# Kernel tuning notes

Hardware: AMD Instinct MI355X
Metric: run time of the kernel (lower is better)

Reference implementation:

```python
import jax, jax.numpy as jnp
import numpy as np

N_NODES_PER_SLICE = 1024  # n_physical_qubits + 1


def _gcn_layer(x, row, col, n_nodes, W, b):
    """PyG GCNConv: add self-loops, symmetric deg normalization, linear, scatter-add, +bias."""
    sl = jnp.arange(n_nodes, dtype=row.dtype)
    row_f = jnp.concatenate([row, sl])
    col_f = jnp.concatenate([col, sl])
    deg = jax.ops.segment_sum(jnp.ones_like(col_f, dtype=x.dtype), col_f, num_segments=n_nodes)
    dinv = jnp.where(deg > 0, jax.lax.rsqrt(deg), 0.0)
    norm = dinv[row_f] * dinv[col_f]            # [E_total]
    h = x @ W                                    # [n_nodes, out]
    msg = h[row_f] * norm[:, None]               # gather + scale
    out = jax.ops.segment_sum(msg, col_f, num_segments=n_nodes)  # scatter-add
    return out + b


def reference(edge_index, qubit_embeddings, W1, b1, W2, b2, W3, b3):
    B = edge_index.shape[0]
    npn = N_NODES_PER_SLICE
    n_nodes = B * npn
    # Batch.from_data_list: offset each slice's edge_index by b * npn, tile node features
    offsets = (jnp.arange(B, dtype=edge_index.dtype) * npn)[:, None]  # [B,1]
    row = (edge_index[:, 0, :] + offsets).reshape(-1)  # [B*E]
    col = (edge_index[:, 1, :] + offsets).reshape(-1)
    x = jnp.tile(qubit_embeddings, (B, 1))             # [B*npn, d0]
    for W, b in ((W1, b1), (W2, b2), (W3, b3)):
        x = jax.nn.relu(_gcn_layer(x, row, col, n_nodes, W, b))
    return x


def setup_inputs() -> dict:
    key = jax.random.key(0)
    ks = jax.random.split(key, 8)
    B, E, d = 512, 2048, 128
    return {
        "edge_index": jax.random.randint(ks[0], (B, 2, E), 0, N_NODES_PER_SLICE, dtype=jnp.int64 if jax.config.jax_enable_x64 else jnp.int32),
        "qubit_embeddings": jax.random.normal(ks[1], (N_NODES_PER_SLICE, d), dtype=jnp.float32),
        "W1": jax.random.normal(ks[2], (d, d), dtype=jnp.float32) * (1.0 / np.sqrt(d)),
        "b1": jnp.zeros((d,), dtype=jnp.float32),
        "W2": jax.random.normal(ks[3], (d, d), dtype=jnp.float32) * (1.0 / np.sqrt(d)),
        "b2": jnp.zeros((d,), dtype=jnp.float32),
        "W3": jax.random.normal(ks[4], (d, d), dtype=jnp.float32) * (1.0 / np.sqrt(d)),
        "b3": jnp.zeros((d,), dtype=jnp.float32),
    }
```

## Files before the change

### kernel.cpp

```cpp
#include <hip/hip_runtime.h>

#define NPN   1024
#define NB    512
#define NE_S  2048
#define DD    128
#define NN    (NB * NPN)
#define NE    (NB * NE_S)

typedef short s16x8 __attribute__((ext_vector_type(8)));
typedef float f32x4 __attribute__((ext_vector_type(4)));

static __device__ __forceinline__ unsigned short f2bf(float f) {
    unsigned u = __builtin_bit_cast(unsigned, f);
    unsigned r = (u + 0x7FFFu + ((u >> 16) & 1u)) >> 16;
    return (unsigned short)r;
}
static __device__ __forceinline__ float bf2f(unsigned short h) {
    unsigned u = ((unsigned)h) << 16;
    return __builtin_bit_cast(float, u);
}


__global__ void k_count(const int* __restrict__ ei, int* __restrict__ deg) {
    int t = blockIdx.x * 256 + threadIdx.x;
    int b = t >> 11, e = t & (NE_S - 1);
    int col = ei[b * (2 * NE_S) + NE_S + e];
    atomicAdd(&deg[b * NPN + col], 1);
}

__global__ void k_dinv(const int* __restrict__ deg, float* __restrict__ dinv) {
    int i = blockIdx.x * 256 + threadIdx.x;
    dinv[i] = rsqrtf((float)(deg[i] + 1));
}

__global__ __launch_bounds__(1024) void k_scan(const int* __restrict__ deg,
                                               int* __restrict__ coff,
                                               int* __restrict__ cur) {
    __shared__ int s[NPN];
    int b = blockIdx.x, t = threadIdx.x;
    int v = deg[b * NPN + t];
    s[t] = v;
    __syncthreads();
    for (int off = 1; off < NPN; off <<= 1) {
        int add = (t >= off) ? s[t - off] : 0;
        __syncthreads();
        s[t] += add;
        __syncthreads();
    }
    coff[b * NPN + t] = b * NE_S + (s[t] - v);
    cur[b * NPN + t] = 0;
}

__global__ void k_fill(const int* __restrict__ ei, const float* __restrict__ dinv,
                       const int* __restrict__ coff, int* __restrict__ cur,
                       int* __restrict__ crow, float* __restrict__ cnorm) {
    int t = blockIdx.x * 256 + threadIdx.x;
    int b = t >> 11, e = t & (NE_S - 1);
    int r = ei[b * (2 * NE_S) + e];
    int c = ei[b * (2 * NE_S) + NE_S + e];
    int gr = b * NPN + r, gc = b * NPN + c;
    int pos = coff[gc] + atomicAdd(&cur[gc], 1);
    crow[pos]  = gr;
    cnorm[pos] = dinv[gr] * dinv[gc];
}


__global__ __launch_bounds__(256) void k_wsplit(const float* __restrict__ W,
                                                short* __restrict__ WTh,
                                                short* __restrict__ WTl) {
    int idx = blockIdx.x * 256 + threadIdx.x;
    int k = idx >> 7, n = idx & 127;
    float f = W[idx];
    unsigned short h = f2bf(f);
    unsigned short l = f2bf(f - bf2f(h));
    WTh[n * DD + k] = (short)h;
    WTl[n * DD + k] = (short)l;
}


__global__ __launch_bounds__(512, 4) void k_layer(const float* __restrict__ x,
                                                  unsigned gmask,
                                                  const short* __restrict__ WTh,
                                                  const short* __restrict__ WTl,
                                                  const float* __restrict__ bias,
                                                  const float* __restrict__ dinv,
                                                  const int* __restrict__ coff,
                                                  const int* __restrict__ deg,
                                                  const int* __restrict__ crow,
                                                  const float* __restrict__ cnorm,
                                                  float* __restrict__ out) {
    __shared__ short sH[128 * DD];
    __shared__ short sL[128 * DD];

    int t = threadIdx.x;
    int wave = t >> 6, lane = t & 63;
    int wb = (int)((blockIdx.x & 7) * 512 + (blockIdx.x >> 3));
    int m0 = wb * 128;

    int n  = lane & 15;
    int kq = lane >> 4;

    const short* bhp = &WTh[(wave * 16 + n) * DD + kq * 8];
    const short* blp = &WTl[(wave * 16 + n) * DD + kq * 8];
    s16x8 bh[4], bl[4];
    #pragma unroll
    for (int ks = 0; ks < 4; ++ks) {
        bh[ks] = *(const s16x8*)(bhp + ks * 32);
        bl[ks] = *(const s16x8*)(blp + ks * 32);
    }

    for (int i = 0; i < 16; ++i) {
        int row = wave * 16 + i;
        int g = m0 + row;
        float dv = dinv[g];
        float2 v = *(const float2*)&x[(size_t)(g & gmask) * DD + lane * 2];
        float ax = dv * dv * v.x, ay = dv * dv * v.y;
        int beg = coff[g], cnt = deg[g];
        for (int e = 0; e < cnt; ++e) {
            int r = crow[beg + e];
            float nw = cnorm[beg + e];
            float2 rv = *(const float2*)&x[(size_t)(r & gmask) * DD + lane * 2];
            ax += nw * rv.x; ay += nw * rv.y;
        }
        unsigned short hx = f2bf(ax); unsigned short lx = f2bf(ax - bf2f(hx));
        unsigned short hy = f2bf(ay); unsigned short ly = f2bf(ay - bf2f(hy));
        unsigned hwrd = ((unsigned)hy << 16) | hx;
        unsigned lwrd = ((unsigned)ly << 16) | lx;
        unsigned bo = ((unsigned)row * 256u + (unsigned)lane * 4u) ^ ((unsigned)(row & 7) << 4);
        *(unsigned*)((char*)sH + bo) = hwrd;
        *(unsigned*)((char*)sL + bo) = lwrd;
    }
    __syncthreads();

    f32x4 acc[8];
    #pragma unroll
    for (int m = 0; m < 8; ++m) acc[m] = (f32x4){0.f, 0.f, 0.f, 0.f};

    #pragma unroll
    for (int ks = 0; ks < 4; ++ks) {
        #pragma unroll
        for (int m = 0; m < 8; ++m) {
            int row = m * 16 + n;
            unsigned bo = ((unsigned)row * 256u + (unsigned)(ks * 64 + kq * 16))
                          ^ ((unsigned)(row & 7) << 4);
            s16x8 ah = *(const s16x8*)((const char*)sH + bo);
            s16x8 al = *(const s16x8*)((const char*)sL + bo);
            acc[m] = __builtin_amdgcn_mfma_f32_16x16x32_bf16(ah, bh[ks], acc[m], 0, 0, 0);
            acc[m] = __builtin_amdgcn_mfma_f32_16x16x32_bf16(ah, bl[ks], acc[m], 0, 0, 0);
            acc[m] = __builtin_amdgcn_mfma_f32_16x16x32_bf16(al, bh[ks], acc[m], 0, 0, 0);
            acc[m] = __builtin_amdgcn_mfma_f32_16x16x32_bf16(al, bl[ks], acc[m], 0, 0, 0);
        }
    }

    int col = wave * 16 + n;
    float bv = bias[col];
    #pragma unroll
    for (int m = 0; m < 8; ++m) {
        #pragma unroll
        for (int r = 0; r < 4; ++r) {
            int row = m * 16 + kq * 4 + r;
            float vv = acc[m][r] + bv;
            out[(size_t)(m0 + row) * DD + col] = fmaxf(vv, 0.f);
        }
    }
}


extern "C" void kernel_launch(void* const* d_in, const int* in_sizes, int n_in,
                              void* d_out, int out_size, void* d_ws, size_t ws_size,
                              hipStream_t stream) {
    const int*   ei  = (const int*)d_in[0];
    const float* emb = (const float*)d_in[1];
    const float* W1  = (const float*)d_in[2];
    const float* b1  = (const float*)d_in[3];
    const float* W2  = (const float*)d_in[4];
    const float* b2  = (const float*)d_in[5];
    const float* W3  = (const float*)d_in[6];
    const float* b3  = (const float*)d_in[7];
    float* out = (float*)d_out;

    float* x_mid = (float*)d_ws;
    float* dinv  = x_mid + (size_t)NN * DD;
    int*   deg   = (int*)(dinv + NN);
    int*   coff  = deg + NN;
    int*   cur   = coff + NN;
    int*   crow  = cur + NN;
    float* cnorm = (float*)(crow + NE);
    short* WTh1  = (short*)(cnorm + NE);
    short* WTl1  = WTh1 + DD * DD;
    short* WTh2  = WTl1 + DD * DD;
    short* WTl2  = WTh2 + DD * DD;
    short* WTh3  = WTl2 + DD * DD;
    short* WTl3  = WTh3 + DD * DD;

    hipMemsetAsync(deg, 0, NN * sizeof(int), stream);
    k_count<<<NE / 256, 256, 0, stream>>>(ei, deg);
    k_dinv<<<NN / 256, 256, 0, stream>>>(deg, dinv);
    k_scan<<<NB, NPN, 0, stream>>>(deg, coff, cur);
    k_fill<<<NE / 256, 256, 0, stream>>>(ei, dinv, coff, cur, crow, cnorm);

    k_wsplit<<<64, 256, 0, stream>>>(W1, WTh1, WTl1);
    k_wsplit<<<64, 256, 0, stream>>>(W2, WTh2, WTl2);
    k_wsplit<<<64, 256, 0, stream>>>(W3, WTh3, WTl3);

    k_layer<<<NN / 128, 512, 0, stream>>>(emb, NPN - 1, WTh1, WTl1, b1,
                                          dinv, coff, deg, crow, cnorm, out);
    k_layer<<<NN / 128, 512, 0, stream>>>(out, 0xFFFFFFFFu, WTh2, WTl2, b2,
                                          dinv, coff, deg, crow, cnorm, x_mid);
    k_layer<<<NN / 128, 512, 0, stream>>>(x_mid, 0xFFFFFFFFu, WTh3, WTl3, b3,
                                          dinv, coff, deg, crow, cnorm, out);
}
```

Measured before the change: 1.095 ms.

## Balance edge aggregation across waves with shared-memory atomics and drop low-low MFMA

Instead of each wave walking the CSR lists of its own 16 destination rows, whose length varies, the block's edge range is split evenly across its 8 waves. Each wave gathers source rows in batches of 8 with shuffled indices and accumulates into an fp32 tile in shared memory using LDS atomics. The shared buffer is then reused for the split-bf16 tiles. The al*bl MFMA term is dropped, cutting matrix work by a quarter at a small cost in precision. The change fixes load imbalance and exposes more loads in flight, at the price of LDS atomic contention and extra barriers.

```diff
diff --git a/kernel.cpp b/kernel.cpp
--- a/kernel.cpp
+++ b/kernel.cpp
@@ -53,14 +53,14 @@
 
 __global__ void k_fill(const int* __restrict__ ei, const float* __restrict__ dinv,
                        const int* __restrict__ coff, int* __restrict__ cur,
-                       int* __restrict__ crow, float* __restrict__ cnorm) {
+                       int2* __restrict__ csd, float* __restrict__ cnorm) {
     int t = blockIdx.x * 256 + threadIdx.x;
     int b = t >> 11, e = t & (NE_S - 1);
     int r = ei[b * (2 * NE_S) + e];
     int c = ei[b * (2 * NE_S) + NE_S + e];
     int gr = b * NPN + r, gc = b * NPN + c;
     int pos = coff[gc] + atomicAdd(&cur[gc], 1);
-    crow[pos]  = gr;
+    csd[pos]   = make_int2(gr, gc);
     cnorm[pos] = dinv[gr] * dinv[gc];
 }
 
@@ -85,12 +85,13 @@
                                                   const float* __restrict__ bias,
                                                   const float* __restrict__ dinv,
                                                   const int* __restrict__ coff,
-                                                  const int* __restrict__ deg,
-                                                  const int* __restrict__ crow,
+                                                  const int2* __restrict__ csd,
                                                   const float* __restrict__ cnorm,
                                                   float* __restrict__ out) {
-    __shared__ short sH[128 * DD];
-    __shared__ short sL[128 * DD];
+    __shared__ float sBuf[128 * DD];
+    float* sAcc = sBuf;
+    char*  sH   = (char*)sBuf;
+    char*  sL   = (char*)sBuf + 32768;
 
     int t = threadIdx.x;
     int wave = t >> 6, lane = t & 63;
@@ -109,26 +110,75 @@
         bl[ks] = *(const s16x8*)(blp + ks * 32);
     }
 
+    #pragma unroll 2
+    for (int h = 0; h < 2; ++h) {
+        float2 sv[8]; float dvv[8];
+        #pragma unroll
+        for (int i = 0; i < 8; ++i) {
+            int row = wave * 16 + h * 8 + i;
+            int g = m0 + row;
+            dvv[i] = dinv[g];
+            sv[i] = *(const float2*)&x[(size_t)((unsigned)g & gmask) * DD + lane * 2];
+        }
+        #pragma unroll
+        for (int i = 0; i < 8; ++i) {
+            int row = wave * 16 + h * 8 + i;
+            float s = dvv[i] * dvv[i];
+            sAcc[row * DD + lane]      = s * sv[i].x;
+            sAcc[row * DD + 64 + lane] = s * sv[i].y;
+        }
+    }
+    __syncthreads();
+
+    int cb0 = coff[m0];
+    int cb1 = (m0 + 128 < NN) ? coff[m0 + 128] : NE;
+    int Eb  = cb1 - cb0;
+    int eBeg = cb0 + (Eb * wave) / 8;
+    int eEnd = cb0 + (Eb * (wave + 1)) / 8;
+
+    for (int c0 = eBeg; c0 < eEnd; c0 += 64) {
+        int nC = min(64, eEnd - c0);
+        int2 sd = make_int2(m0, m0); float nw = 0.f;
+        if (lane < nC) { sd = csd[c0 + lane]; nw = cnorm[c0 + lane]; }
+        for (int b0 = 0; b0 < nC; b0 += 8) {
+            float2 v[8]; int dl[8]; float wj[8];
+            int nB = min(8, nC - b0);
+            #pragma unroll
+            for (int j = 0; j < 8; ++j) {
+                if (j < nB) {
+                    int src = __shfl(sd.x, b0 + j);
+                    dl[j]   = __shfl(sd.y, b0 + j) - m0;
+                    wj[j]   = __shfl(nw,   b0 + j);
+                    v[j] = *(const float2*)&x[(size_t)((unsigned)src & gmask) * DD + lane * 2];
+                }
+            }
+            #pragma unroll
+            for (int j = 0; j < 8; ++j) {
+                if (j < nB) {
+                    atomicAdd(&sAcc[dl[j] * DD + lane],      wj[j] * v[j].x);
+                    atomicAdd(&sAcc[dl[j] * DD + 64 + lane], wj[j] * v[j].y);
+                }
+            }
+        }
+    }
+    __syncthreads();
+
+    float fe[16], fo[16];
+    #pragma unroll
     for (int i = 0; i < 16; ++i) {
         int row = wave * 16 + i;
-        int g = m0 + row;
-        float dv = dinv[g];
-        float2 v = *(const float2*)&x[(size_t)(g & gmask) * DD + lane * 2];
-        float ax = dv * dv * v.x, ay = dv * dv * v.y;
-        int beg = coff[g], cnt = deg[g];
-        for (int e = 0; e < cnt; ++e) {
-            int r = crow[beg + e];
-            float nw = cnorm[beg + e];
-            float2 rv = *(const float2*)&x[(size_t)(r & gmask) * DD + lane * 2];
-            ax += nw * rv.x; ay += nw * rv.y;
-        }
-        unsigned short hx = f2bf(ax); unsigned short lx = f2bf(ax - bf2f(hx));
-        unsigned short hy = f2bf(ay); unsigned short ly = f2bf(ay - bf2f(hy));
-        unsigned hwrd = ((unsigned)hy << 16) | hx;
-        unsigned lwrd = ((unsigned)ly << 16) | lx;
+        fe[i] = sAcc[row * DD + lane];
+        fo[i] = sAcc[row * DD + 64 + lane];
+    }
+    __syncthreads();
+    #pragma unroll
+    for (int i = 0; i < 16; ++i) {
+        int row = wave * 16 + i;
+        unsigned short hx = f2bf(fe[i]); unsigned short lx = f2bf(fe[i] - bf2f(hx));
+        unsigned short hy = f2bf(fo[i]); unsigned short ly = f2bf(fo[i] - bf2f(hy));
         unsigned bo = ((unsigned)row * 256u + (unsigned)lane * 4u) ^ ((unsigned)(row & 7) << 4);
-        *(unsigned*)((char*)sH + bo) = hwrd;
-        *(unsigned*)((char*)sL + bo) = lwrd;
+        *(unsigned*)(sH + bo) = ((unsigned)hy << 16) | hx;
+        *(unsigned*)(sL + bo) = ((unsigned)ly << 16) | lx;
     }
     __syncthreads();
 
@@ -143,12 +193,11 @@
             int row = m * 16 + n;
             unsigned bo = ((unsigned)row * 256u + (unsigned)(ks * 64 + kq * 16))
                           ^ ((unsigned)(row & 7) << 4);
-            s16x8 ah = *(const s16x8*)((const char*)sH + bo);
-            s16x8 al = *(const s16x8*)((const char*)sL + bo);
+            s16x8 ah = *(const s16x8*)(sH + bo);
+            s16x8 al = *(const s16x8*)(sL + bo);
             acc[m] = __builtin_amdgcn_mfma_f32_16x16x32_bf16(ah, bh[ks], acc[m], 0, 0, 0);
             acc[m] = __builtin_amdgcn_mfma_f32_16x16x32_bf16(ah, bl[ks], acc[m], 0, 0, 0);
             acc[m] = __builtin_amdgcn_mfma_f32_16x16x32_bf16(al, bh[ks], acc[m], 0, 0, 0);
-            acc[m] = __builtin_amdgcn_mfma_f32_16x16x32_bf16(al, bl[ks], acc[m], 0, 0, 0);
         }
     }
 
@@ -184,8 +233,8 @@
     int*   deg   = (int*)(dinv + NN);
     int*   coff  = deg + NN;
     int*   cur   = coff + NN;
-    int*   crow  = cur + NN;
-    float* cnorm = (float*)(crow + NE);
+    int2*  csd   = (int2*)(cur + NN);
+    float* cnorm = (float*)(csd + NE);
     short* WTh1  = (short*)(cnorm + NE);
     short* WTl1  = WTh1 + DD * DD;
     short* WTh2  = WTl1 + DD * DD;
@@ -197,16 +246,16 @@
     k_count<<<NE / 256, 256, 0, stream>>>(ei, deg);
     k_dinv<<<NN / 256, 256, 0, stream>>>(deg, dinv);
     k_scan<<<NB, NPN, 0, stream>>>(deg, coff, cur);
-    k_fill<<<NE / 256, 256, 0, stream>>>(ei, dinv, coff, cur, crow, cnorm);
+    k_fill<<<NE / 256, 256, 0, stream>>>(ei, dinv, coff, cur, csd, cnorm);
 
     k_wsplit<<<64, 256, 0, stream>>>(W1, WTh1, WTl1);
     k_wsplit<<<64, 256, 0, stream>>>(W2, WTh2, WTl2);
     k_wsplit<<<64, 256, 0, stream>>>(W3, WTh3, WTl3);
 
     k_layer<<<NN / 128, 512, 0, stream>>>(emb, NPN - 1, WTh1, WTl1, b1,
-                                          dinv, coff, deg, crow, cnorm, out);
+                                          dinv, coff, csd, cnorm, out);
     k_layer<<<NN / 128, 512, 0, stream>>>(out, 0xFFFFFFFFu, WTh2, WTl2, b2,
-                                          dinv, coff, deg, crow, cnorm, x_mid);
+                                          dinv, coff, csd, cnorm, x_mid);
     k_layer<<<NN / 128, 512, 0, stream>>>(x_mid, 0xFFFFFFFFu, WTh3, WTl3, b3,
-                                          dinv, coff, deg, crow, cnorm, out);
-}
+                                          dinv, coff, csd, cnorm, out);
+}
```

Result: slower. 2.515 ms (+129.7%).
